# Optimization experiments

Hardware: AMD Instinct MI355X
Metric: run time of the kernel (lower is better)

## Reference

```python
import jax, jax.numpy as jnp
import numpy as np

B, S, D, K = 4, 2048, 1024, 8

def setup_inputs() -> dict:
    key = jax.random.key(0)
    k1, k2, k3 = jax.random.split(key, 3)
    hidden_states = jax.random.normal(k1, (B, S, D), dtype=jnp.float32)
    # scaled so scores ~ O(1) and exp() does not overflow
    W_phi = jax.random.normal(k2, (D, D), dtype=jnp.float32) * 0.005
    W_psi = jax.random.normal(k3, (D, D), dtype=jnp.float32) * 0.005
    return {"hidden_states": hidden_states, "W_phi": W_phi, "W_psi": W_psi, "k": K}

def reference(hidden_states, W_phi, W_psi, k):
    b, s, d = hidden_states.shape
    k = min(k, s)
    # nn.Linear(bias=False): y = x @ W.T
    phi_h = hidden_states @ W_phi.T            # [b,s,d]
    psi_h = hidden_states @ W_psi.T            # [b,s,d]
    scores = jnp.einsum('bsd,btd->bst', phi_h, psi_h)  # [b,s,s]
    affinity = jnp.exp(scores)
    topk_values, topk_indices = jax.lax.top_k(affinity, k)   # [b,s,k]
    norm_sum = topk_values.sum(axis=-1, keepdims=True) + 1e-8
    normalized_weights = topk_values / norm_sum
    batch_offset = (jnp.arange(b) * s)[:, None, None]        # [b,1,1]
    src_local = jnp.arange(s)[None, :, None]                 # [1,s,1]
    src_global = jnp.broadcast_to(batch_offset + src_local, (b, s, k))
    dst_global = batch_offset + topk_indices
    mask = (topk_indices != src_local).reshape(-1)           # drop self-loops
    # eager boolean compaction (data-dependent size, like the torch module)
    src_final = src_global.reshape(-1)[mask]
    dst_final = dst_global.reshape(-1)[mask]
    weights_final = normalized_weights.reshape(-1)[mask]
    if src_final.size == 0:
        all_nodes = jnp.arange(b * s)
        return jnp.stack([all_nodes, all_nodes], axis=0), jnp.ones(b * s, dtype=jnp.float32)
    edge_index = jnp.stack([src_final, dst_final], axis=0)
    return edge_index, weights_final
```

## Files before the change

kernel.cpp:

```cpp
#include <hip/hip_runtime.h>
#include <cmath>

#define SEQ 2048
#define DDIM 1024
#define NROWS 8192
#define KSEL 8
#define IMAXC 0x7fffffff

typedef __attribute__((ext_vector_type(8))) short bf16x8;
typedef __attribute__((ext_vector_type(4))) float f32x4;
typedef __attribute__((ext_vector_type(4))) double f64x4;

__device__ __forceinline__ unsigned short f2bf(float f) {
  unsigned u = __builtin_bit_cast(unsigned, f);
  u = (u + 0x7fffu + ((u >> 16) & 1u)) >> 16;
  return (unsigned short)u;
}
__device__ __forceinline__ float bf2f(unsigned short h) {
  unsigned u = ((unsigned)h) << 16;
  return __builtin_bit_cast(float, u);
}
__device__ __forceinline__ unsigned pkbf(float a, float b) {
  unsigned r;
  asm("v_cvt_pk_bf16_f32 %0, %1, %2" : "=v"(r) : "v"(a), "v"(b));
  return r;
}
__device__ __forceinline__ void dmap(int sel, int lg, int lr, int rg,
                                     int& ri, int& ci) {
  switch (sel) {
    case 0:  ri = (lg << 2) + rg; ci = lr; break;
    case 1:  ri = lg + (rg << 2); ci = lr; break;
    case 2:  ri = lr; ci = (lg << 2) + rg; break;
    default: ri = lr; ci = lg + (rg << 2); break;
  }
}

__global__ void kprobe(int* __restrict__ sel) {
  const int lane = threadIdx.x;
  const int lr = lane & 15, lg = lane >> 4;
  const double a = (double)(4 * lr + lg + 1);
  const double b = (double)(9 * lr + 5 * lg + 2);
  f64x4 d = (f64x4){0.0, 0.0, 0.0, 0.0};
  d = __builtin_amdgcn_mfma_f64_16x16x4f64(a, b, d, 0, 0, 0);
  int my = 4;
  for (int s = 3; s >= 0; --s) {
    bool ok = true;
    for (int rg = 0; rg < 4; ++rg) {
      int ri, ci;
      dmap(s, lg, lr, rg, ri, ci);
      double e = 0.0;
      for (int k = 0; k < 4; ++k)
        e += (double)(4 * ri + k + 1) * (double)(9 * ci + 5 * k + 2);
      ok = ok && (d[rg] == e);
    }
    if (__all(ok)) my = s;
  }
  if (lane == 0) sel[0] = my;
}

__global__ __launch_bounds__(256, 2)
void k0_mfma(const float* __restrict__ A, const float* __restrict__ B,
             float* __restrict__ C, const int* __restrict__ selp) {
  const int sel = selp[0];
  if (sel >= 4) return;
  __shared__ float As[32][72];
  __shared__ float Bs[32][72];
  const int tid = threadIdx.x;
  const int lane = tid & 63, w = tid >> 6;
  const int wr = w >> 1, wc = w & 1;
  const int lr = lane & 15, lg = lane >> 4;
  const int brow = blockIdx.y << 6, bcol = blockIdx.x << 6;
  const int kr = tid >> 3, c4 = (tid & 7) << 2;

  f64x4 acc[2][2];
#pragma unroll
  for (int mi = 0; mi < 2; ++mi)
#pragma unroll
    for (int nj = 0; nj < 2; ++nj)
      acc[mi][nj] = (f64x4){0.0, 0.0, 0.0, 0.0};

  const float* Ap = &A[(size_t)kr * DDIM + brow + c4];
  const float* Bp = &B[(size_t)kr * DDIM + bcol + c4];
  float4 pa0 = *reinterpret_cast<const float4*>(Ap);
  float4 pa1 = *reinterpret_cast<const float4*>(Ap + 32);
  float4 pb0 = *reinterpret_cast<const float4*>(Bp);
  float4 pb1 = *reinterpret_cast<const float4*>(Bp + 32);

  for (int k0 = 0; k0 < DDIM; k0 += 32) {
    __syncthreads();
    *reinterpret_cast<float4*>(&As[kr][c4]) = pa0;
    *reinterpret_cast<float4*>(&As[kr][c4 + 32]) = pa1;
    *reinterpret_cast<float4*>(&Bs[kr][c4]) = pb0;
    *reinterpret_cast<float4*>(&Bs[kr][c4 + 32]) = pb1;
    __syncthreads();
    if (k0 + 32 < DDIM) {
      const size_t nk = (size_t)(k0 + 32) * DDIM;
      pa0 = *reinterpret_cast<const float4*>(Ap + nk);
      pa1 = *reinterpret_cast<const float4*>(Ap + nk + 32);
      pb0 = *reinterpret_cast<const float4*>(Bp + nk);
      pb1 = *reinterpret_cast<const float4*>(Bp + nk + 32);
    }
#pragma unroll
    for (int kp = 0; kp < 8; ++kp) {
      const int ka = (kp << 2) + lg;
      double a[2], b[2];
#pragma unroll
      for (int mi = 0; mi < 2; ++mi)
        a[mi] = (double)As[ka][(wr << 5) + (mi << 4) + lr];
#pragma unroll
      for (int nj = 0; nj < 2; ++nj)
        b[nj] = (double)Bs[ka][(wc << 5) + (nj << 4) + lr];
#pragma unroll
      for (int mi = 0; mi < 2; ++mi)
#pragma unroll
        for (int nj = 0; nj < 2; ++nj)
          acc[mi][nj] = __builtin_amdgcn_mfma_f64_16x16x4f64(
              a[mi], b[nj], acc[mi][nj], 0, 0, 0);
    }
  }
#pragma unroll
  for (int mi = 0; mi < 2; ++mi)
#pragma unroll
    for (int nj = 0; nj < 2; ++nj)
#pragma unroll
      for (int rg = 0; rg < 4; ++rg) {
        int ri, ci;
        dmap(sel, lg, lr, rg, ri, ci);
        C[(size_t)(brow + (wr << 5) + (mi << 4) + ri) * DDIM +
          bcol + (wc << 5) + (nj << 4) + ci] = (float)acc[mi][nj][rg];
      }
}

__global__ __launch_bounds__(256)
void k0_repair(const float* __restrict__ A, const float* __restrict__ B,
               float* __restrict__ C, const int* __restrict__ selp) {
  if (selp[0] < 4) return;
  __shared__ __align__(16) float As[32][68];
  __shared__ __align__(16) float Bs[32][68];
  const int tid = threadIdx.x;
  const int tx = tid & 15, ty = tid >> 4;
  const int brow = blockIdx.y << 6;
  const int bcol = blockIdx.x << 6;
  double acc[4][4] = {};
  for (int k0 = 0; k0 < DDIM; k0 += 32) {
#pragma unroll
    for (int i = 0; i < 2; ++i) {
      const int f = tid + (i << 8);
      const int r = f >> 4;
      const int c4 = (f & 15) << 2;
      *reinterpret_cast<float4*>(&As[r][c4]) =
          *reinterpret_cast<const float4*>(&A[(size_t)(k0 + r) * DDIM + brow + c4]);
      *reinterpret_cast<float4*>(&Bs[r][c4]) =
          *reinterpret_cast<const float4*>(&B[(size_t)(k0 + r) * DDIM + bcol + c4]);
    }
    __syncthreads();
#pragma unroll
    for (int kk = 0; kk < 32; ++kk) {
      const float4 a = *reinterpret_cast<const float4*>(&As[kk][ty << 2]);
      const float4 b = *reinterpret_cast<const float4*>(&Bs[kk][tx << 2]);
      const double ad[4] = {a.x, a.y, a.z, a.w};
      const double bd[4] = {b.x, b.y, b.z, b.w};
#pragma unroll
      for (int i = 0; i < 4; ++i)
#pragma unroll
        for (int j = 0; j < 4; ++j)
          acc[i][j] = fma(ad[i], bd[j], acc[i][j]);
    }
    __syncthreads();
  }
#pragma unroll
  for (int i = 0; i < 4; ++i) {
    float4 v = make_float4((float)acc[i][0], (float)acc[i][1],
                           (float)acc[i][2], (float)acc[i][3]);
    *reinterpret_cast<float4*>(
        &C[(size_t)(brow + (ty << 2) + i) * DDIM + bcol + (tx << 2)]) = v;
  }
}

#define K1_STAGE(bi)                                              \
  do {                                                            \
    As[bi][akh + 0][ar] = pa0.x; As[bi][akh + 1][ar] = pa0.y;     \
    As[bi][akh + 2][ar] = pa0.z; As[bi][akh + 3][ar] = pa0.w;     \
    As[bi][akh + 4][ar] = pa1.x; As[bi][akh + 5][ar] = pa1.y;     \
    As[bi][akh + 6][ar] = pa1.z; As[bi][akh + 7][ar] = pa1.w;     \
    *reinterpret_cast<float4*>(&Bs[bi][bk][bc4]) = pb0;           \
    *reinterpret_cast<float4*>(&Bs[bi][bk][bc4 + 64]) = pb1;      \
  } while (0)

__global__ __launch_bounds__(256, 2)
void k1_mfma(const float* __restrict__ A, const float* __restrict__ B,
             float* __restrict__ C, const int* __restrict__ selp) {
  const int sel = selp[0];
  if (sel >= 4) return;
  __shared__ float As[2][16][144];
  __shared__ float Bs[2][16][144];
  const int tid = threadIdx.x;
  const int lin = blockIdx.y * 8 + blockIdx.x;
  const int nlin = (lin & 7) * 64 + (lin >> 3);
  const int brow = (nlin >> 3) << 7;
  const int bcol = (nlin & 7) << 7;
  const int lane = tid & 63, w = tid >> 6;
  const int wr = w >> 1, wc = w & 1;
  const int lr = lane & 15, lg = lane >> 4;
  const int ar = tid >> 1, akh = (tid & 1) << 3;
  const int bk = tid >> 4, bc4 = (tid & 15) << 2;

  f64x4 acc[4][4];
#pragma unroll
  for (int mi = 0; mi < 4; ++mi)
#pragma unroll
    for (int nj = 0; nj < 4; ++nj)
      acc[mi][nj] = (f64x4){0.0, 0.0, 0.0, 0.0};

  const float* Ap = &A[(size_t)(brow + ar) * DDIM + akh];
  const float* Bp = &B[(size_t)bk * DDIM + bcol + bc4];

  float4 pa0 = *reinterpret_cast<const float4*>(Ap);
  float4 pa1 = *reinterpret_cast<const float4*>(Ap + 4);
  float4 pb0 = *reinterpret_cast<const float4*>(Bp);
  float4 pb1 = *reinterpret_cast<const float4*>(Bp + 64);
  K1_STAGE(0);
  pa0 = *reinterpret_cast<const float4*>(Ap + 16);
  pa1 = *reinterpret_cast<const float4*>(Ap + 20);
  pb0 = *reinterpret_cast<const float4*>(Bp + (size_t)16 * DDIM);
  pb1 = *reinterpret_cast<const float4*>(Bp + (size_t)16 * DDIM + 64);

  for (int t = 0; t < 64; ++t) {
    __syncthreads();
    const int cur = t & 1;
    if (t < 63) {
      K1_STAGE(cur ^ 1);
      if (t < 62) {
        const size_t ko = (size_t)(t + 2) << 4;
        pa0 = *reinterpret_cast<const float4*>(Ap + ko);
        pa1 = *reinterpret_cast<const float4*>(Ap + ko + 4);
        pb0 = *reinterpret_cast<const float4*>(Bp + ko * DDIM);
        pb1 = *reinterpret_cast<const float4*>(Bp + ko * DDIM + 64);
      }
    }
#pragma unroll
    for (int kp = 0; kp < 4; ++kp) {
      const int ka = (kp << 2) + lg;
      double a[4], b[4];
#pragma unroll
      for (int mi = 0; mi < 4; ++mi)
        a[mi] = (double)As[cur][ka][(wr << 6) + (mi << 4) + lr];
#pragma unroll
      for (int nj = 0; nj < 4; ++nj)
        b[nj] = (double)Bs[cur][ka][(wc << 6) + (nj << 4) + lr];
#pragma unroll
      for (int mi = 0; mi < 4; ++mi)
#pragma unroll
        for (int nj = 0; nj < 4; ++nj)
          acc[mi][nj] = __builtin_amdgcn_mfma_f64_16x16x4f64(
              a[mi], b[nj], acc[mi][nj], 0, 0, 0);
    }
  }
#pragma unroll
  for (int mi = 0; mi < 4; ++mi)
#pragma unroll
    for (int nj = 0; nj < 4; ++nj)
#pragma unroll
      for (int rg = 0; rg < 4; ++rg) {
        int ri, ci;
        dmap(sel, lg, lr, rg, ri, ci);
        C[(size_t)(brow + (wr << 6) + (mi << 4) + ri) * DDIM +
          bcol + (wc << 6) + (nj << 4) + ci] = (float)acc[mi][nj][rg];
      }
}

__global__ __launch_bounds__(256, 2)
void k1_repair(const float* __restrict__ A, const float* __restrict__ B,
               float* __restrict__ C, const int* __restrict__ selp) {
  if (selp[0] < 4) return;
  __shared__ double As[128][17];
  __shared__ double Bs[16][130];
  const int tid = threadIdx.x;
  const int lin = blockIdx.y * 8 + blockIdx.x;
  const int nlin = (lin & 7) * 64 + (lin >> 3);
  const int brow = (nlin >> 3) << 7;
  const int bcol = (nlin & 7) << 7;
  const int tx = tid & 15, ty = tid >> 4;
  const int ar = tid >> 1, aks = (tid & 1) << 3;
  const int bk = tid >> 4, btx = tid & 15;

  double acc[8][8];
#pragma unroll
  for (int i = 0; i < 8; ++i)
#pragma unroll
    for (int j = 0; j < 8; ++j) acc[i][j] = 0.0;

  const float* Aptr = &A[(size_t)(brow + ar) * DDIM + aks];
  const float* Bptr = &B[(size_t)bk * DDIM + bcol + (btx << 1)];

  float4 pa0, pa1;
  float2 pb[4];
  pa0 = *reinterpret_cast<const float4*>(Aptr);
  pa1 = *reinterpret_cast<const float4*>(Aptr + 4);
#pragma unroll
  for (int w = 0; w < 4; ++w)
    pb[w] = *reinterpret_cast<const float2*>(Bptr + (w << 5));

  for (int k0 = 0; k0 < DDIM; k0 += 16) {
    __syncthreads();
    As[ar][aks + 0] = (double)pa0.x; As[ar][aks + 1] = (double)pa0.y;
    As[ar][aks + 2] = (double)pa0.z; As[ar][aks + 3] = (double)pa0.w;
    As[ar][aks + 4] = (double)pa1.x; As[ar][aks + 5] = (double)pa1.y;
    As[ar][aks + 6] = (double)pa1.z; As[ar][aks + 7] = (double)pa1.w;
#pragma unroll
    for (int w = 0; w < 4; ++w) {
      Bs[bk][(btx << 1) + (w << 5) + 0] = (double)pb[w].x;
      Bs[bk][(btx << 1) + (w << 5) + 1] = (double)pb[w].y;
    }
    __syncthreads();
    if (k0 + 16 < DDIM) {
      pa0 = *reinterpret_cast<const float4*>(Aptr + k0 + 16);
      pa1 = *reinterpret_cast<const float4*>(Aptr + k0 + 20);
#pragma unroll
      for (int w = 0; w < 4; ++w)
        pb[w] = *reinterpret_cast<const float2*>(
            Bptr + (size_t)(k0 + 16) * DDIM + (w << 5));
    }
#pragma unroll 8
    for (int kk = 0; kk < 16; ++kk) {
      double a[8];
      double2 b[4];
#pragma unroll
      for (int i = 0; i < 8; ++i) a[i] = As[(ty << 3) + i][kk];
#pragma unroll
      for (int jj = 0; jj < 4; ++jj)
        b[jj] = *reinterpret_cast<const double2*>(&Bs[kk][(tx << 1) + (jj << 5)]);
#pragma unroll
      for (int i = 0; i < 8; ++i) {
#pragma unroll
        for (int jj = 0; jj < 4; ++jj) {
          acc[i][(jj << 1) + 0] = fma(a[i], b[jj].x, acc[i][(jj << 1) + 0]);
          acc[i][(jj << 1) + 1] = fma(a[i], b[jj].y, acc[i][(jj << 1) + 1]);
        }
      }
    }
  }
#pragma unroll
  for (int i = 0; i < 8; ++i) {
    float* crow = &C[(size_t)(brow + (ty << 3) + i) * DDIM + bcol + (tx << 1)];
#pragma unroll
    for (int jj = 0; jj < 4; ++jj) {
      float2 v = make_float2((float)acc[i][(jj << 1)],
                             (float)acc[i][(jj << 1) + 1]);
      *reinterpret_cast<float2*>(crow + (jj << 5)) = v;
    }
  }
}

__global__ __launch_bounds__(256)
void k2_mfma(const float* __restrict__ T, const float* __restrict__ H,
             unsigned short* __restrict__ cand_v,
             unsigned char* __restrict__ cand_i) {
  __shared__ union {
    unsigned short stage[2][128 * 64];
    float Sl[64][130];
    struct {
      float mv[256][8];
      unsigned char mi[256][8];
    } mg;
  } u;
  const int tid = threadIdx.x;
  const int lane = tid & 63;
  const int w = tid >> 6;
  const int wr = w >> 1, wc = w & 1;
  const int lr = lane & 15, lg = lane >> 4;
  const int z = blockIdx.z;
  const int brow = blockIdx.y << 7, bcol = blockIdx.x << 7;
  const int row0g = z * SEQ + brow;
  const int col0g = z * SEQ + bcol;

  f32x4 acc[4][4];
#pragma unroll
  for (int mi = 0; mi < 4; ++mi)
#pragma unroll
    for (int nj = 0; nj < 4; ++nj)
      acc[mi][nj] = (f32x4){0.f, 0.f, 0.f, 0.f};

  for (int k0 = 0; k0 < DDIM; k0 += 64) {
    __syncthreads();
#pragma unroll
    for (int q = 0; q < 4; ++q) {
      const int c = (q << 8) + tid;
      const int row = c >> 3, slot = c & 7;
      const int gs = slot ^ (row & 7);
      {
        const float* s = &T[(size_t)(row0g + row) * DDIM + k0 + (gs << 3)];
        const float4 f0 = *reinterpret_cast<const float4*>(s);
        const float4 f1 = *reinterpret_cast<const float4*>(s + 4);
        uint4 o;
        o.x = pkbf(f0.x, f0.y); o.y = pkbf(f0.z, f0.w);
        o.z = pkbf(f1.x, f1.y); o.w = pkbf(f1.z, f1.w);
        *reinterpret_cast<uint4*>(&u.stage[0][c << 3]) = o;
      }
      {
        const float* s = &H[(size_t)(col0g + row) * DDIM + k0 + (gs << 3)];
        const float4 f0 = *reinterpret_cast<const float4*>(s);
        const float4 f1 = *reinterpret_cast<const float4*>(s + 4);
        uint4 o;
        o.x = pkbf(f0.x, f0.y); o.y = pkbf(f0.z, f0.w);
        o.z = pkbf(f1.x, f1.y); o.w = pkbf(f1.z, f1.w);
        *reinterpret_cast<uint4*>(&u.stage[1][c << 3]) = o;
      }
    }
    __syncthreads();
#pragma unroll
    for (int kh = 0; kh < 2; ++kh) {
      bf16x8 af[4], bf[4];
      const int sl = (kh << 2) + lg;
#pragma unroll
      for (int mi = 0; mi < 4; ++mi) {
        const int ra = (wr << 6) + (mi << 4) + lr;
        af[mi] = *reinterpret_cast<const bf16x8*>(
            &u.stage[0][(ra << 6) + ((sl ^ (ra & 7)) << 3)]);
        const int rb = (wc << 6) + (mi << 4) + lr;
        bf[mi] = *reinterpret_cast<const bf16x8*>(
            &u.stage[1][(rb << 6) + ((sl ^ (rb & 7)) << 3)]);
      }
#pragma unroll
      for (int mi = 0; mi < 4; ++mi)
#pragma unroll
        for (int nj = 0; nj < 4; ++nj)
          acc[mi][nj] = __builtin_amdgcn_mfma_f32_16x16x32_bf16(
              af[mi], bf[nj], acc[mi][nj], 0, 0, 0);
    }
  }

  const int bx = blockIdx.x;
  const int srow = tid >> 2;
  const int qd = tid & 3;
  for (int p = 0; p < 2; ++p) {
    __syncthreads();
    if (wr == p) {
#pragma unroll
      for (int mi = 0; mi < 4; ++mi)
#pragma unroll
        for (int nj = 0; nj < 4; ++nj)
#pragma unroll
          for (int r = 0; r < 4; ++r)
            u.Sl[(mi << 4) + (lg << 2) + r][(wc << 6) + (nj << 4) + lr] =
                acc[mi][nj][r];
    }
    __syncthreads();
    float v[KSEL];
    int ci[KSEL];
#pragma unroll
    for (int s = 0; s < KSEL; ++s) { v[s] = -3.0e38f; ci[s] = 0; }
    const int c0 = qd << 5;
    for (int c = 0; c < 32; ++c) {
      const float x = u.Sl[srow][c0 + c];
      if (x > v[KSEL - 1]) {
        float pv = x; int pc = c0 + c;
#pragma unroll
        for (int s = 0; s < KSEL; ++s) {
          if (x > v[s]) {
            const float tv = v[s]; const int tc = ci[s];
            v[s] = pv; ci[s] = pc; pv = tv; pc = tc;
          }
        }
      }
    }
    __syncthreads();
#pragma unroll
    for (int s = 0; s < KSEL; ++s) {
      u.mg.mv[tid][s] = v[s];
      u.mg.mi[tid][s] = (unsigned char)ci[s];
    }
    __syncthreads();
    if (qd == 0) {
      float fv[KSEL];
      int fi[KSEL];
#pragma unroll
      for (int s = 0; s < KSEL; ++s) { fv[s] = -3.0e38f; fi[s] = 0; }
#pragma unroll
      for (int t = 0; t < 4; ++t) {
#pragma unroll
        for (int s = 0; s < KSEL; ++s) {
          const float x = u.mg.mv[tid + t][s];
          const int idx = u.mg.mi[tid + t][s];
          if (x > fv[KSEL - 1]) {
            float pv = x; int pc = idx;
#pragma unroll
            for (int s2 = 0; s2 < KSEL; ++s2) {
              if (x > fv[s2]) {
                const float tv = fv[s2]; const int tc = fi[s2];
                fv[s2] = pv; fi[s2] = pc; pv = tv; pc = tc;
              }
            }
          }
        }
      }
      const size_t base =
          (size_t)(row0g + (p << 6) + srow) * 128 + ((size_t)bx << 3);
#pragma unroll
      for (int s = 0; s < KSEL; ++s) {
        cand_v[base + s] = f2bf(fv[s]);
        cand_i[base + s] = (unsigned char)fi[s];
      }
    }
  }
}

__global__ __launch_bounds__(256)
void kr_rescore(const float* __restrict__ T, const float* __restrict__ H,
                const unsigned short* __restrict__ cand_v,
                const unsigned char* __restrict__ cand_i,
                int* __restrict__ topi, float* __restrict__ topw,
                int* __restrict__ cnt) {
  const int tid = threadIdx.x, lane = tid & 63, w = tid >> 6;
  const int r = blockIdx.x * 4 + w;
  const int b = r >> 11, iloc = r & (SEQ - 1);

  const size_t cbase = (size_t)r * 128;
  const int s0 = lane << 1, s1 = s0 + 1;
  float v0 = bf2f(cand_v[cbase + s0]);
  float v1 = bf2f(cand_v[cbase + s1]);
  int i0 = ((s0 >> 3) << 7) + cand_i[cbase + s0];
  int i1 = ((s1 >> 3) << 7) + cand_i[cbase + s1];
  if (v1 > v0) {
    const float tv = v0; v0 = v1; v1 = tv;
    const int ti = i0; i0 = i1; i1 = ti;
  }
  int keep = 0;
  for (int rnd = 0; rnd < 16; ++rnd) {
    float m = v0;
#pragma unroll
    for (int off = 32; off >= 1; off >>= 1) m = fmaxf(m, __shfl_xor(m, off));
    const unsigned long long bm = __ballot(v0 == m);
    const int owner = __ffsll(bm) - 1;
    const int oi = __shfl(i0, owner);
    if (lane == owner) { v0 = v1; i0 = i1; v1 = -3.0e38f; }
    if (lane == rnd) keep = oi;
  }

  const float* Trow = T + (size_t)r * DDIM;
  float4 t4[4];
#pragma unroll
  for (int q = 0; q < 4; ++q)
    t4[q] = *reinterpret_cast<const float4*>(&Trow[(q << 8) + (lane << 2)]);

  float t8v[KSEL];
  int t8i[KSEL];
#pragma unroll
  for (int p = 0; p < KSEL; ++p) { t8v[p] = -1.0f; t8i[p] = IMAXC; }

  for (int c = 0; c < 16; ++c) {
    const int j = __shfl(keep, c);
    const float* Hrow = H + ((size_t)(b << 11) + j) * DDIM;
    double s = 0.0;
#pragma unroll
    for (int q = 0; q < 4; ++q) {
      const float4 h = *reinterpret_cast<const float4*>(&Hrow[(q << 8) + (lane << 2)]);
      s = fma((double)t4[q].x, (double)h.x, s);
      s = fma((double)t4[q].y, (double)h.y, s);
      s = fma((double)t4[q].z, (double)h.z, s);
      s = fma((double)t4[q].w, (double)h.w, s);
    }
#pragma unroll
    for (int off = 1; off < 64; off <<= 1) s += __shfl_xor(s, off);
    const float aff = expf((float)s);
    const bool g7 = (aff > t8v[KSEL - 1]) ||
                    (aff == t8v[KSEL - 1] && j < t8i[KSEL - 1]);
    if (g7) {
      float pv = aff; int pi = j;
#pragma unroll
      for (int p = 0; p < KSEL; ++p) {
        const bool g = (aff > t8v[p]) || (aff == t8v[p] && j < t8i[p]);
        if (g) {
          const float tv = t8v[p]; const int ti = t8i[p];
          t8v[p] = pv; t8i[p] = pi; pv = tv; pi = ti;
        }
      }
    }
  }
  if (lane == 0) {
    float sum = 0.0f;
#pragma unroll
    for (int p = 0; p < KSEL; ++p) sum += t8v[p];
    sum += 1e-8f;
    int c8 = KSEL;
#pragma unroll
    for (int p = 0; p < KSEL; ++p)
      if (t8i[p] == iloc) --c8;
    cnt[r] = c8;
#pragma unroll
    for (int p = 0; p < KSEL; ++p) {
      topi[(size_t)r * KSEL + p] = t8i[p];
      topw[(size_t)r * KSEL + p] = t8v[p] / sum;
    }
  }
}

__global__ __launch_bounds__(1024)
void k4_scan(const int* __restrict__ cnt, int* __restrict__ off) {
  __shared__ int part[1024];
  const int t = threadIdx.x;
  int loc[8];
  int s = 0;
#pragma unroll
  for (int i = 0; i < 8; ++i) { loc[i] = s; s += cnt[t * 8 + i]; }
  part[t] = s;
  __syncthreads();
  for (int d = 1; d < 1024; d <<= 1) {
    const int add = (t >= d) ? part[t - d] : 0;
    __syncthreads();
    part[t] += add;
    __syncthreads();
  }
  const int base = (t == 0) ? 0 : part[t - 1];
#pragma unroll
  for (int i = 0; i < 8; ++i) off[t * 8 + i] = base + loc[i];
}

__global__ __launch_bounds__(256)
void k5_emit(const int* __restrict__ topi, const float* __restrict__ topw,
             const int* __restrict__ off, float* __restrict__ out, int E) {
  const int r = blockIdx.x * 256 + threadIdx.x;
  if (r >= NROWS) return;
  const int o = off[r];
  const int sloc = r & (SEQ - 1);
  const int bbase = r & ~(SEQ - 1);
  int e = 0;
#pragma unroll
  for (int p = 0; p < KSEL; ++p) {
    const int id = topi[(size_t)r * KSEL + p];
    const float w = topw[(size_t)r * KSEL + p];
    if (id != sloc) {
      const int pos = o + e;
      if (pos < E) {
        out[pos] = (float)r;
        out[(size_t)E + pos] = (float)(bbase + id);
        out[2 * (size_t)E + pos] = w;
      }
      ++e;
    }
  }
}

extern "C" void kernel_launch(void* const* d_in, const int* in_sizes, int n_in,
                              void* d_out, int out_size, void* d_ws,
                              size_t ws_size, hipStream_t stream) {
  const float* H = (const float*)d_in[0];
  const float* Wphi = (const float*)d_in[1];
  const float* Wpsi = (const float*)d_in[2];
  float* out = (float*)d_out;
  const int E = out_size / 3;

  char* base = (char*)d_ws;
  float* T = (float*)base;
  char* regionX = base + 33554432;
  float* Wc = (float*)regionX;
  unsigned short* cand_v = (unsigned short*)regionX;
  unsigned char* cand_i = (unsigned char*)(regionX + 2097152);
  char* pp = regionX + 4194304;
  int* topi = (int*)pp;  pp += 262144;
  float* topw = (float*)pp; pp += 262144;
  int* cnt = (int*)pp;   pp += 32768;
  int* off = (int*)pp;   pp += 32768;
  int* sel = (int*)pp;

  kprobe<<<dim3(1), 64, 0, stream>>>(sel);
  k0_mfma<<<dim3(16, 16), 256, 0, stream>>>(Wphi, Wpsi, Wc, sel);
  k0_repair<<<dim3(16, 16), 256, 0, stream>>>(Wphi, Wpsi, Wc, sel);
  k1_mfma<<<dim3(8, 64), 256, 0, stream>>>(H, Wc, T, sel);
  k1_repair<<<dim3(8, 64), 256, 0, stream>>>(H, Wc, T, sel);
  k2_mfma<<<dim3(16, 16, 4), 256, 0, stream>>>(T, H, cand_v, cand_i);
  kr_rescore<<<dim3(NROWS / 4), 256, 0, stream>>>(T, H, cand_v, cand_i,
                                                  topi, topw, cnt);
  k4_scan<<<dim3(1), 1024, 0, stream>>>(cnt, off);
  k5_emit<<<dim3(NROWS / 256), 256, 0, stream>>>(topi, topw, off, out, E);
}
```

Before: 601.2 us.

## Pre-convert T and H to bf16 for candidate GEMM; parallelize rescore dot products

Adds a conversion kernel that writes bf16 copies of T and H once. The candidate-scoring GEMM then stages bf16 tiles straight from global memory instead of converting fp32 on the fly, which cuts its load bandwidth in half. The rescore kernel now computes all 16 candidate dot products at once, using four lanes per candidate, instead of running 16 sequential full-wave reductions. This path runs only when the workspace is large enough, and it costs an extra pass over T and H plus more workspace.

```diff
diff --git a/kernel.cpp b/kernel.cpp
--- a/kernel.cpp
+++ b/kernel.cpp
@@ -348,6 +348,173 @@
       float2 v = make_float2((float)acc[i][(jj << 1)],
                              (float)acc[i][(jj << 1) + 1]);
       *reinterpret_cast<float2*>(crow + (jj << 5)) = v;
+    }
+  }
+}
+
+__global__ __launch_bounds__(256)
+void kcvt2(const float* __restrict__ Tin, const float* __restrict__ Hin,
+           unsigned short* __restrict__ Tb, unsigned short* __restrict__ Hb) {
+  const size_t i = ((size_t)blockIdx.x * 256 + threadIdx.x) << 3;
+  {
+    const float4 a0 = *reinterpret_cast<const float4*>(&Tin[i]);
+    const float4 a1 = *reinterpret_cast<const float4*>(&Tin[i + 4]);
+    uint4 o;
+    o.x = pkbf(a0.x, a0.y); o.y = pkbf(a0.z, a0.w);
+    o.z = pkbf(a1.x, a1.y); o.w = pkbf(a1.z, a1.w);
+    *reinterpret_cast<uint4*>(&Tb[i]) = o;
+  }
+  {
+    const float4 a0 = *reinterpret_cast<const float4*>(&Hin[i]);
+    const float4 a1 = *reinterpret_cast<const float4*>(&Hin[i + 4]);
+    uint4 o;
+    o.x = pkbf(a0.x, a0.y); o.y = pkbf(a0.z, a0.w);
+    o.z = pkbf(a1.x, a1.y); o.w = pkbf(a1.z, a1.w);
+    *reinterpret_cast<uint4*>(&Hb[i]) = o;
+  }
+}
+
+__global__ __launch_bounds__(256)
+void k2_mfma_bf(const unsigned short* __restrict__ Tb,
+                const unsigned short* __restrict__ Hb,
+                unsigned short* __restrict__ cand_v,
+                unsigned char* __restrict__ cand_i) {
+  __shared__ union {
+    unsigned short stage[2][128 * 64];
+    float Sl[64][130];
+    struct {
+      float mv[256][8];
+      unsigned char mi[256][8];
+    } mg;
+  } u;
+  const int tid = threadIdx.x;
+  const int lane = tid & 63;
+  const int w = tid >> 6;
+  const int wr = w >> 1, wc = w & 1;
+  const int lr = lane & 15, lg = lane >> 4;
+  const int lin = blockIdx.z * 256 + blockIdx.y * 16 + blockIdx.x;
+  const int nl = (lin & 7) * 128 + (lin >> 3);
+  const int bx = nl & 15;
+  const int by = (nl >> 4) & 15;
+  const int bz = nl >> 8;
+  const int brow = by << 7, bcol = bx << 7;
+  const int row0g = bz * SEQ + brow;
+  const int col0g = bz * SEQ + bcol;
+
+  f32x4 acc[4][4];
+#pragma unroll
+  for (int mi = 0; mi < 4; ++mi)
+#pragma unroll
+    for (int nj = 0; nj < 4; ++nj)
+      acc[mi][nj] = (f32x4){0.f, 0.f, 0.f, 0.f};
+
+  for (int k0 = 0; k0 < DDIM; k0 += 64) {
+    __syncthreads();
+#pragma unroll
+    for (int q = 0; q < 4; ++q) {
+      const int c = (q << 8) + tid;
+      const int row = c >> 3, slot = c & 7;
+      const int gs = slot ^ (row & 7);
+      *reinterpret_cast<uint4*>(&u.stage[0][c << 3]) =
+          *reinterpret_cast<const uint4*>(
+              &Tb[(size_t)(row0g + row) * DDIM + k0 + (gs << 3)]);
+      *reinterpret_cast<uint4*>(&u.stage[1][c << 3]) =
+          *reinterpret_cast<const uint4*>(
+              &Hb[(size_t)(col0g + row) * DDIM + k0 + (gs << 3)]);
+    }
+    __syncthreads();
+#pragma unroll
+    for (int kh = 0; kh < 2; ++kh) {
+      bf16x8 af[4], bf[4];
+      const int sl = (kh << 2) + lg;
+#pragma unroll
+      for (int mi = 0; mi < 4; ++mi) {
+        const int ra = (wr << 6) + (mi << 4) + lr;
+        af[mi] = *reinterpret_cast<const bf16x8*>(
+            &u.stage[0][(ra << 6) + ((sl ^ (ra & 7)) << 3)]);
+        const int rb = (wc << 6) + (mi << 4) + lr;
+        bf[mi] = *reinterpret_cast<const bf16x8*>(
+            &u.stage[1][(rb << 6) + ((sl ^ (rb & 7)) << 3)]);
+      }
+#pragma unroll
+      for (int mi = 0; mi < 4; ++mi)
+#pragma unroll
+        for (int nj = 0; nj < 4; ++nj)
+          acc[mi][nj] = __builtin_amdgcn_mfma_f32_16x16x32_bf16(
+              af[mi], bf[nj], acc[mi][nj], 0, 0, 0);
+    }
+  }
+
+  const int srow = tid >> 2;
+  const int qd = tid & 3;
+  for (int p = 0; p < 2; ++p) {
+    __syncthreads();
+    if (wr == p) {
+#pragma unroll
+      for (int mi = 0; mi < 4; ++mi)
+#pragma unroll
+        for (int nj = 0; nj < 4; ++nj)
+#pragma unroll
+          for (int r = 0; r < 4; ++r)
+            u.Sl[(mi << 4) + (lg << 2) + r][(wc << 6) + (nj << 4) + lr] =
+                acc[mi][nj][r];
+    }
+    __syncthreads();
+    float v[KSEL];
+    int ci[KSEL];
+#pragma unroll
+    for (int s = 0; s < KSEL; ++s) { v[s] = -3.0e38f; ci[s] = 0; }
+    const int c0 = qd << 5;
+    for (int c = 0; c < 32; ++c) {
+      const float x = u.Sl[srow][c0 + c];
+      if (x > v[KSEL - 1]) {
+        float pv = x; int pc = c0 + c;
+#pragma unroll
+        for (int s = 0; s < KSEL; ++s) {
+          if (x > v[s]) {
+            const float tv = v[s]; const int tc = ci[s];
+            v[s] = pv; ci[s] = pc; pv = tv; pc = tc;
+          }
+        }
+      }
+    }
+    __syncthreads();
+#pragma unroll
+    for (int s = 0; s < KSEL; ++s) {
+      u.mg.mv[tid][s] = v[s];
+      u.mg.mi[tid][s] = (unsigned char)ci[s];
+    }
+    __syncthreads();
+    if (qd == 0) {
+      float fv[KSEL];
+      int fi[KSEL];
+#pragma unroll
+      for (int s = 0; s < KSEL; ++s) { fv[s] = -3.0e38f; fi[s] = 0; }
+#pragma unroll
+      for (int t = 0; t < 4; ++t) {
+#pragma unroll
+        for (int s = 0; s < KSEL; ++s) {
+          const float x = u.mg.mv[tid + t][s];
+          const int idx = u.mg.mi[tid + t][s];
+          if (x > fv[KSEL - 1]) {
+            float pv = x; int pc = idx;
+#pragma unroll
+            for (int s2 = 0; s2 < KSEL; ++s2) {
+              if (x > fv[s2]) {
+                const float tv = fv[s2]; const int tc = fi[s2];
+                fv[s2] = pv; fi[s2] = pc; pv = tv; pc = tc;
+              }
+            }
+          }
+        }
+      }
+      const size_t base =
+          (size_t)(row0g + (p << 6) + srow) * 128 + ((size_t)bx << 3);
+#pragma unroll
+      for (int s = 0; s < KSEL; ++s) {
+        cand_v[base + s] = f2bf(fv[s]);
+        cand_i[base + s] = (unsigned char)fi[s];
+      }
     }
   }
 }
@@ -537,42 +704,41 @@
     if (lane == rnd) keep = oi;
   }
 
-  const float* Trow = T + (size_t)r * DDIM;
-  float4 t4[4];
-#pragma unroll
-  for (int q = 0; q < 4; ++q)
-    t4[q] = *reinterpret_cast<const float4*>(&Trow[(q << 8) + (lane << 2)]);
+  const int g = lane >> 2, p = lane & 3;
+  const int jg = __shfl(keep, g);
+  const float* Trow = T + (size_t)r * DDIM + (p << 8);
+  const float* Hrow = H + ((size_t)(b << 11) + jg) * DDIM + (p << 8);
+  double s = 0.0;
+#pragma unroll 4
+  for (int q = 0; q < 64; ++q) {
+    const float4 tv = *reinterpret_cast<const float4*>(Trow + (q << 2));
+    const float4 hv = *reinterpret_cast<const float4*>(Hrow + (q << 2));
+    s = fma((double)tv.x, (double)hv.x, s);
+    s = fma((double)tv.y, (double)hv.y, s);
+    s = fma((double)tv.z, (double)hv.z, s);
+    s = fma((double)tv.w, (double)hv.w, s);
+  }
+  s += __shfl_xor(s, 1);
+  s += __shfl_xor(s, 2);
+  const float aff = expf((float)s);
 
   float t8v[KSEL];
   int t8i[KSEL];
 #pragma unroll
-  for (int p = 0; p < KSEL; ++p) { t8v[p] = -1.0f; t8i[p] = IMAXC; }
-
+  for (int q = 0; q < KSEL; ++q) { t8v[q] = -1.0f; t8i[q] = IMAXC; }
   for (int c = 0; c < 16; ++c) {
-    const int j = __shfl(keep, c);
-    const float* Hrow = H + ((size_t)(b << 11) + j) * DDIM;
-    double s = 0.0;
-#pragma unroll
-    for (int q = 0; q < 4; ++q) {
-      const float4 h = *reinterpret_cast<const float4*>(&Hrow[(q << 8) + (lane << 2)]);
-      s = fma((double)t4[q].x, (double)h.x, s);
-      s = fma((double)t4[q].y, (double)h.y, s);
-      s = fma((double)t4[q].z, (double)h.z, s);
-      s = fma((double)t4[q].w, (double)h.w, s);
-    }
-#pragma unroll
-    for (int off = 1; off < 64; off <<= 1) s += __shfl_xor(s, off);
-    const float aff = expf((float)s);
-    const bool g7 = (aff > t8v[KSEL - 1]) ||
-                    (aff == t8v[KSEL - 1] && j < t8i[KSEL - 1]);
+    const float ac = __shfl(aff, c << 2);
+    const int jc = __shfl(keep, c);
+    const bool g7 = (ac > t8v[KSEL - 1]) ||
+                    (ac == t8v[KSEL - 1] && jc < t8i[KSEL - 1]);
     if (g7) {
-      float pv = aff; int pi = j;
-#pragma unroll
-      for (int p = 0; p < KSEL; ++p) {
-        const bool g = (aff > t8v[p]) || (aff == t8v[p] && j < t8i[p]);
-        if (g) {
-          const float tv = t8v[p]; const int ti = t8i[p];
-          t8v[p] = pv; t8i[p] = pi; pv = tv; pi = ti;
+      float pv = ac; int pi = jc;
+#pragma unroll
+      for (int q = 0; q < KSEL; ++q) {
+        const bool gi = (ac > t8v[q]) || (ac == t8v[q] && jc < t8i[q]);
+        if (gi) {
+          const float tv = t8v[q]; const int ti = t8i[q];
+          t8v[q] = pv; t8i[q] = pi; pv = tv; pi = ti;
         }
       }
     }
@@ -580,17 +746,17 @@
   if (lane == 0) {
     float sum = 0.0f;
 #pragma unroll
-    for (int p = 0; p < KSEL; ++p) sum += t8v[p];
+    for (int q = 0; q < KSEL; ++q) sum += t8v[q];
     sum += 1e-8f;
     int c8 = KSEL;
 #pragma unroll
-    for (int p = 0; p < KSEL; ++p)
-      if (t8i[p] == iloc) --c8;
+    for (int q = 0; q < KSEL; ++q)
+      if (t8i[q] == iloc) --c8;
     cnt[r] = c8;
 #pragma unroll
-    for (int p = 0; p < KSEL; ++p) {
-      topi[(size_t)r * KSEL + p] = t8i[p];
-      topw[(size_t)r * KSEL + p] = t8v[p] / sum;
+    for (int q = 0; q < KSEL; ++q) {
+      topi[(size_t)r * KSEL + q] = t8i[q];
+      topw[(size_t)r * KSEL + q] = t8v[q] / sum;
     }
   }
 }
@@ -649,28 +815,56 @@
   const float* Wpsi = (const float*)d_in[2];
   float* out = (float*)d_out;
   const int E = out_size / 3;
-
   char* base = (char*)d_ws;
-  float* T = (float*)base;
-  char* regionX = base + 33554432;
-  float* Wc = (float*)regionX;
-  unsigned short* cand_v = (unsigned short*)regionX;
-  unsigned char* cand_i = (unsigned char*)(regionX + 2097152);
-  char* pp = regionX + 4194304;
-  int* topi = (int*)pp;  pp += 262144;
-  float* topw = (float*)pp; pp += 262144;
-  int* cnt = (int*)pp;   pp += 32768;
-  int* off = (int*)pp;   pp += 32768;
-  int* sel = (int*)pp;
-
-  kprobe<<<dim3(1), 64, 0, stream>>>(sel);
-  k0_mfma<<<dim3(16, 16), 256, 0, stream>>>(Wphi, Wpsi, Wc, sel);
-  k0_repair<<<dim3(16, 16), 256, 0, stream>>>(Wphi, Wpsi, Wc, sel);
-  k1_mfma<<<dim3(8, 64), 256, 0, stream>>>(H, Wc, T, sel);
-  k1_repair<<<dim3(8, 64), 256, 0, stream>>>(H, Wc, T, sel);
-  k2_mfma<<<dim3(16, 16, 4), 256, 0, stream>>>(T, H, cand_v, cand_i);
-  kr_rescore<<<dim3(NROWS / 4), 256, 0, stream>>>(T, H, cand_v, cand_i,
-                                                  topi, topw, cnt);
-  k4_scan<<<dim3(1), 1024, 0, stream>>>(cnt, off);
-  k5_emit<<<dim3(NROWS / 256), 256, 0, stream>>>(topi, topw, off, out, E);
-}
+
+  const size_t NEED_FAST = 70844420;
+  if (ws_size >= NEED_FAST) {
+    float* T = (float*)base;
+    unsigned short* Hb = (unsigned short*)(base + 33554432);
+    char* tbwc = base + 50331648;
+    float* Wc = (float*)tbwc;
+    unsigned short* Tb = (unsigned short*)tbwc;
+    unsigned short* cand_v = (unsigned short*)(base + 67108864);
+    unsigned char* cand_i = (unsigned char*)(base + 69206016);
+    int* topi = (int*)(base + 70254592);
+    float* topw = (float*)(base + 70516736);
+    int* cnt = (int*)(base + 70778880);
+    int* off = (int*)(base + 70811648);
+    int* sel = (int*)(base + 70844416);
+
+    kprobe<<<dim3(1), 64, 0, stream>>>(sel);
+    k0_mfma<<<dim3(16, 16), 256, 0, stream>>>(Wphi, Wpsi, Wc, sel);
+    k0_repair<<<dim3(16, 16), 256, 0, stream>>>(Wphi, Wpsi, Wc, sel);
+    k1_mfma<<<dim3(8, 64), 256, 0, stream>>>(H, Wc, T, sel);
+    k1_repair<<<dim3(8, 64), 256, 0, stream>>>(H, Wc, T, sel);
+    kcvt2<<<dim3(4096), 256, 0, stream>>>(T, H, Tb, Hb);
+    k2_mfma_bf<<<dim3(16, 16, 4), 256, 0, stream>>>(Tb, Hb, cand_v, cand_i);
+    kr_rescore<<<dim3(NROWS / 4), 256, 0, stream>>>(T, H, cand_v, cand_i,
+                                                    topi, topw, cnt);
+    k4_scan<<<dim3(1), 1024, 0, stream>>>(cnt, off);
+    k5_emit<<<dim3(NROWS / 256), 256, 0, stream>>>(topi, topw, off, out, E);
+  } else {
+    float* T = (float*)base;
+    char* regionX = base + 33554432;
+    float* Wc = (float*)regionX;
+    unsigned short* cand_v = (unsigned short*)regionX;
+    unsigned char* cand_i = (unsigned char*)(regionX + 2097152);
+    char* pp = regionX + 4194304;
+    int* topi = (int*)pp;  pp += 262144;
+    float* topw = (float*)pp; pp += 262144;
+    int* cnt = (int*)pp;   pp += 32768;
+    int* off = (int*)pp;   pp += 32768;
+    int* sel = (int*)pp;
+
+    kprobe<<<dim3(1), 64, 0, stream>>>(sel);
+    k0_mfma<<<dim3(16, 16), 256, 0, stream>>>(Wphi, Wpsi, Wc, sel);
+    k0_repair<<<dim3(16, 16), 256, 0, stream>>>(Wphi, Wpsi, Wc, sel);
+    k1_mfma<<<dim3(8, 64), 256, 0, stream>>>(H, Wc, T, sel);
+    k1_repair<<<dim3(8, 64), 256, 0, stream>>>(H, Wc, T, sel);
+    k2_mfma<<<dim3(16, 16, 4), 256, 0, stream>>>(T, H, cand_v, cand_i);
+    kr_rescore<<<dim3(NROWS / 4), 256, 0, stream>>>(T, H, cand_v, cand_i,
+                                                    topi, topw, cnt);
+    k4_scan<<<dim3(1), 1024, 0, stream>>>(cnt, off);
+    k5_emit<<<dim3(NROWS / 256), 256, 0, stream>>>(topi, topw, off, out, E);
+  }
+}
```

After: 644.9 us. 7.3% more time.

## Enlarge score-GEMM tiles to 256x256 with 512 threads and fewer candidates

Applied to the files above, without the earlier changes.

The score GEMM kernel moves from 128x128 tiles with 256 threads to 256x256 tiles with 512 threads (8 waves in a 2x4 layout). Each tile staged from global and converted to bf16 is therefore reused across more outputs, cutting redundant loads and conversions of T and H. The per-row top-8 candidates are now kept per 256-column block (64 per row instead of 128), which simplifies the rescore kernel's selection to one candidate per lane. The cost is a large LDS footprint (64 KB staging) and more accumulator registers, giving one block per CU and only 128 blocks total. That may leave some of the device's CUs idle.

```diff
diff --git a/kernel.cpp b/kernel.cpp
--- a/kernel.cpp
+++ b/kernel.cpp
@@ -352,31 +352,32 @@
   }
 }
 
-__global__ __launch_bounds__(256)
+__global__ __launch_bounds__(512, 1)
 void k2_mfma(const float* __restrict__ T, const float* __restrict__ H,
              unsigned short* __restrict__ cand_v,
              unsigned char* __restrict__ cand_i) {
   __shared__ union {
-    unsigned short stage[2][128 * 64];
-    float Sl[64][130];
+    unsigned short stage[2][256 * 64];
+    float Sl[64][264];
     struct {
-      float mv[256][8];
-      unsigned char mi[256][8];
+      float mv[512][8];
+      unsigned char mi[512][8];
     } mg;
   } u;
   const int tid = threadIdx.x;
   const int lane = tid & 63;
   const int w = tid >> 6;
-  const int wr = w >> 1, wc = w & 1;
+  const int wr = w >> 2, wc = w & 3;
   const int lr = lane & 15, lg = lane >> 4;
   const int z = blockIdx.z;
-  const int brow = blockIdx.y << 7, bcol = blockIdx.x << 7;
+  const int bx = blockIdx.x;
+  const int brow = blockIdx.y << 8, bcol = bx << 8;
   const int row0g = z * SEQ + brow;
   const int col0g = z * SEQ + bcol;
 
-  f32x4 acc[4][4];
-#pragma unroll
-  for (int mi = 0; mi < 4; ++mi)
+  f32x4 acc[8][4];
+#pragma unroll
+  for (int mi = 0; mi < 8; ++mi)
 #pragma unroll
     for (int nj = 0; nj < 4; ++nj)
       acc[mi][nj] = (f32x4){0.f, 0.f, 0.f, 0.f};
@@ -385,7 +386,7 @@
     __syncthreads();
 #pragma unroll
     for (int q = 0; q < 4; ++q) {
-      const int c = (q << 8) + tid;
+      const int c = (q << 9) + tid;
       const int row = c >> 3, slot = c & 7;
       const int gs = slot ^ (row & 7);
       {
@@ -410,40 +411,42 @@
     __syncthreads();
 #pragma unroll
     for (int kh = 0; kh < 2; ++kh) {
-      bf16x8 af[4], bf[4];
       const int sl = (kh << 2) + lg;
-#pragma unroll
-      for (int mi = 0; mi < 4; ++mi) {
-        const int ra = (wr << 6) + (mi << 4) + lr;
-        af[mi] = *reinterpret_cast<const bf16x8*>(
+      bf16x8 bfv[4];
+#pragma unroll
+      for (int nj = 0; nj < 4; ++nj) {
+        const int rb = (wc << 6) + (nj << 4) + lr;
+        bfv[nj] = *reinterpret_cast<const bf16x8*>(
+            &u.stage[1][(rb << 6) + ((sl ^ (rb & 7)) << 3)]);
+      }
+#pragma unroll
+      for (int mi = 0; mi < 8; ++mi) {
+        const int ra = (wr << 7) + (mi << 4) + lr;
+        const bf16x8 af = *reinterpret_cast<const bf16x8*>(
             &u.stage[0][(ra << 6) + ((sl ^ (ra & 7)) << 3)]);
-        const int rb = (wc << 6) + (mi << 4) + lr;
-        bf[mi] = *reinterpret_cast<const bf16x8*>(
-            &u.stage[1][(rb << 6) + ((sl ^ (rb & 7)) << 3)]);
-      }
-#pragma unroll
-      for (int mi = 0; mi < 4; ++mi)
 #pragma unroll
         for (int nj = 0; nj < 4; ++nj)
           acc[mi][nj] = __builtin_amdgcn_mfma_f32_16x16x32_bf16(
-              af[mi], bf[nj], acc[mi][nj], 0, 0, 0);
-    }
-  }
-
-  const int bx = blockIdx.x;
-  const int srow = tid >> 2;
-  const int qd = tid & 3;
-  for (int p = 0; p < 2; ++p) {
-    __syncthreads();
-    if (wr == p) {
-#pragma unroll
-      for (int mi = 0; mi < 4; ++mi)
+              af, bfv[nj], acc[mi][nj], 0, 0, 0);
+      }
+    }
+  }
+
+  const int srow = tid >> 3;
+  const int qd = tid & 7;
+#pragma unroll
+  for (int p = 0; p < 4; ++p) {
+    __syncthreads();
+    if (wr == (p >> 1)) {
+      const int mib = (p & 1) << 2;
+#pragma unroll
+      for (int mi2 = 0; mi2 < 4; ++mi2)
 #pragma unroll
         for (int nj = 0; nj < 4; ++nj)
 #pragma unroll
-          for (int r = 0; r < 4; ++r)
-            u.Sl[(mi << 4) + (lg << 2) + r][(wc << 6) + (nj << 4) + lr] =
-                acc[mi][nj][r];
+          for (int rg = 0; rg < 4; ++rg)
+            u.Sl[(mi2 << 4) + (lg << 2) + rg][(wc << 6) + (nj << 4) + lr] =
+                acc[mib + mi2][nj][rg];
     }
     __syncthreads();
     float v[KSEL];
@@ -477,7 +480,7 @@
 #pragma unroll
       for (int s = 0; s < KSEL; ++s) { fv[s] = -3.0e38f; fi[s] = 0; }
 #pragma unroll
-      for (int t = 0; t < 4; ++t) {
+      for (int t = 0; t < 8; ++t) {
 #pragma unroll
         for (int s = 0; s < KSEL; ++s) {
           const float x = u.mg.mv[tid + t][s];
@@ -495,7 +498,7 @@
         }
       }
       const size_t base =
-          (size_t)(row0g + (p << 6) + srow) * 128 + ((size_t)bx << 3);
+          (size_t)(row0g + (p << 6) + srow) * 64 + ((size_t)bx << 3);
 #pragma unroll
       for (int s = 0; s < KSEL; ++s) {
         cand_v[base + s] = f2bf(fv[s]);
@@ -515,16 +518,9 @@
   const int r = blockIdx.x * 4 + w;
   const int b = r >> 11, iloc = r & (SEQ - 1);
 
-  const size_t cbase = (size_t)r * 128;
-  const int s0 = lane << 1, s1 = s0 + 1;
-  float v0 = bf2f(cand_v[cbase + s0]);
-  float v1 = bf2f(cand_v[cbase + s1]);
-  int i0 = ((s0 >> 3) << 7) + cand_i[cbase + s0];
-  int i1 = ((s1 >> 3) << 7) + cand_i[cbase + s1];
-  if (v1 > v0) {
-    const float tv = v0; v0 = v1; v1 = tv;
-    const int ti = i0; i0 = i1; i1 = ti;
-  }
+  const size_t cbase = (size_t)r * 64;
+  float v0 = bf2f(cand_v[cbase + lane]);
+  int i0 = ((lane >> 3) << 8) + cand_i[cbase + lane];
   int keep = 0;
   for (int rnd = 0; rnd < 16; ++rnd) {
     float m = v0;
@@ -533,7 +529,7 @@
     const unsigned long long bm = __ballot(v0 == m);
     const int owner = __ffsll(bm) - 1;
     const int oi = __shfl(i0, owner);
-    if (lane == owner) { v0 = v1; i0 = i1; v1 = -3.0e38f; }
+    if (lane == owner) v0 = -3.0e38f;
     if (lane == rnd) keep = oi;
   }
 
@@ -668,7 +664,7 @@
   k0_repair<<<dim3(16, 16), 256, 0, stream>>>(Wphi, Wpsi, Wc, sel);
   k1_mfma<<<dim3(8, 64), 256, 0, stream>>>(H, Wc, T, sel);
   k1_repair<<<dim3(8, 64), 256, 0, stream>>>(H, Wc, T, sel);
-  k2_mfma<<<dim3(16, 16, 4), 256, 0, stream>>>(T, H, cand_v, cand_i);
+  k2_mfma<<<dim3(8, 8, 4), 512, 0, stream>>>(T, H, cand_v, cand_i);
   kr_rescore<<<dim3(NROWS / 4), 256, 0, stream>>>(T, H, cand_v, cand_i,
                                                   topi, topw, cnt);
   k4_scan<<<dim3(1), 1024, 0, stream>>>(cnt, off);
```

Result: no change. 592.1 us (-1.5%).
